# Optimization experiments

Hardware: AMD Instinct MI355X
Metric: run time of the kernel (lower is better)

Reference implementation:

```python
import jax, jax.numpy as jnp
import numpy as np

D_MODEL = 1024
D_FF = 4096
N = 16384


def setup_inputs() -> dict:
    key = jax.random.key(0)
    k_b, k_w1, k_b1, k_w2, k_b2 = jax.random.split(key, 5)
    s1 = 1.0 / np.sqrt(D_MODEL)
    s2 = 1.0 / np.sqrt(D_FF)
    return {
        "batch": jax.random.normal(k_b, (N, D_MODEL), dtype=jnp.float32),
        # nn.Linear stores weight as [out_features, in_features]
        "W1": jax.random.uniform(k_w1, (D_FF, D_MODEL), jnp.float32, -s1, s1),
        "b1": jax.random.uniform(k_b1, (D_FF,), jnp.float32, -s1, s1),
        "W2": jax.random.uniform(k_w2, (D_MODEL, D_FF), jnp.float32, -s2, s2),
        "b2": jax.random.uniform(k_b2, (D_MODEL,), jnp.float32, -s2, s2),
    }


def reference(batch, W1, b1, W2, b2):
    # inner = tanh(linear1(batch)) : [N, d_ff]
    inner = jnp.tanh(batch @ W1.T + b1)
    # wx = tanh(linear2(inner)) : [N, d_model]
    wx = jnp.tanh(inner @ W2.T + b2)
    # diag(wx @ batch.T) == row-wise dot product, avoids O(N^2) matmul
    return jax.nn.sigmoid(jnp.sum(wx * batch, axis=-1))  # [N]
```

## Files before the change

### kernel.cpp

```cpp
#include <hip/hip_runtime.h>
#include <math.h>

#define N_ROWS 16384
#define DMODEL 1024
#define DFF    4096

typedef _Float16 f16;
typedef __attribute__((ext_vector_type(4))) _Float16 f16x4;
typedef __attribute__((ext_vector_type(8))) _Float16 f16x8;
typedef __attribute__((ext_vector_type(4))) float f32x4;

__device__ inline void async_ld16(const f16* g, f16* l) {
  __builtin_amdgcn_global_load_lds(
      (__attribute__((address_space(1))) void*)(g),
      (__attribute__((address_space(3))) void*)(l),
      16, 0, 0);
}

__device__ inline float fast_tanh(float x) {
  float t = __expf(2.0f * x);
  return 1.0f - 2.0f / (t + 1.0f);
}

__global__ void cast_to_f16(const float* __restrict__ src, f16* __restrict__ dst, int n) {
  int i = (blockIdx.x * blockDim.x + threadIdx.x) * 8;
  if (i >= n) return;
  float4 v0 = ((const float4*)(src + i))[0];
  float4 v1 = ((const float4*)(src + i))[1];
  f16x8 h = { (f16)v0.x, (f16)v0.y, (f16)v0.z, (f16)v0.w,
              (f16)v1.x, (f16)v1.y, (f16)v1.z, (f16)v1.w };
  *(f16x8*)(dst + i) = h;
}

template <int K>
__global__ __launch_bounds__(256, 3)
void gemm_bt_tanh(const f16* __restrict__ A, const f16* __restrict__ B,
                  const float* __restrict__ bias, f16* __restrict__ C, int Nc) {
  __shared__ __align__(16) f16 As[2 * 128 * 32];
  __shared__ __align__(16) f16 Bs[2 * 128 * 32];

  const int tid  = threadIdx.x;
  const int lane = tid & 63;
  const int wave = tid >> 6;
  const size_t row0 = (size_t)blockIdx.x * 128;
  const size_t col0 = (size_t)blockIdx.y * 128;
  const int wm = (wave >> 1) * 64;
  const int wn = (wave & 1) * 64;
  const int fr = lane & 15;
  const int fk = (lane >> 4) * 8;

  const f16* Ag[4]; const f16* Bg[4]; f16* Asd[4]; f16* Bsd[4];
#pragma unroll
  for (int l = 0; l < 4; ++l) {
    const int sp  = (l & 1) * 256 + tid;
    const int row = sp >> 2;
    const int kch = (l >> 1) * 4 + (sp & 3);
    Ag[l]  = A + (row0 + row) * (size_t)K + kch * 8;
    Bg[l]  = B + (col0 + row) * (size_t)K + kch * 8;
    Asd[l] = As + (l >> 1) * 4096 + sp * 8;
    Bsd[l] = Bs + (l >> 1) * 4096 + sp * 8;
  }

  f32x4 acc[4][4] = {};

  for (int k0 = 0; k0 < K; k0 += 64) {
    __syncthreads();
#pragma unroll
    for (int l = 0; l < 4; ++l) async_ld16(Ag[l] + k0, Asd[l]);
#pragma unroll
    for (int l = 0; l < 4; ++l) async_ld16(Bg[l] + k0, Bsd[l]);
    __syncthreads();

#pragma unroll
    for (int s = 0; s < 2; ++s) {
      f16x8 af[4], bf[4];
#pragma unroll
      for (int i = 0; i < 4; ++i) {
        af[i] = *(const f16x8*)(As + s * 4096 + (wm + i * 16 + fr) * 32 + fk);
        bf[i] = *(const f16x8*)(Bs + s * 4096 + (wn + i * 16 + fr) * 32 + fk);
      }
#pragma unroll
      for (int i = 0; i < 4; ++i)
#pragma unroll
        for (int j = 0; j < 4; ++j)
          acc[i][j] = __builtin_amdgcn_mfma_f32_16x16x32_f16(af[i], bf[j], acc[i][j], 0, 0, 0);
    }
  }

  const int erow = wm + (lane >> 4) * 4;
  const int ecol = wn + fr;
#pragma unroll
  for (int i = 0; i < 4; ++i) {
#pragma unroll
    for (int j = 0; j < 4; ++j) {
      size_t gcol = col0 + ecol + j * 16;
      float b = bias[gcol];
#pragma unroll
      for (int r = 0; r < 4; ++r) {
        size_t grow = row0 + erow + i * 16 + r;
        C[grow * (size_t)Nc + gcol] = (f16)fast_tanh(acc[i][j][r] + b);
      }
    }
  }
}

__global__ void rowdot_sigmoid(const f16* __restrict__ wx, const float* __restrict__ batch,
                               float* __restrict__ out) {
  const int row = blockIdx.x;
  const int t = threadIdx.x;
  const f16* wr = wx + (size_t)row * DMODEL + t * 4;
  const float* br = batch + (size_t)row * DMODEL + t * 4;
  f16x4 h = *(const f16x4*)wr;
  float4 b4 = *(const float4*)br;
  float s = (float)h[0] * b4.x + (float)h[1] * b4.y + (float)h[2] * b4.z + (float)h[3] * b4.w;
#pragma unroll
  for (int off = 32; off > 0; off >>= 1) s += __shfl_down(s, off, 64);
  __shared__ float partial[4];
  if ((t & 63) == 0) partial[t >> 6] = s;
  __syncthreads();
  if (t == 0) {
    float tot = partial[0] + partial[1] + partial[2] + partial[3];
    out[row] = 1.0f / (1.0f + __expf(-tot));
  }
}

extern "C" void kernel_launch(void* const* d_in, const int* in_sizes, int n_in,
                              void* d_out, int out_size, void* d_ws, size_t ws_size,
                              hipStream_t stream) {
  const float* batch = (const float*)d_in[0];
  const float* W1    = (const float*)d_in[1];
  const float* b1    = (const float*)d_in[2];
  const float* W2    = (const float*)d_in[3];
  const float* b2    = (const float*)d_in[4];
  float* out = (float*)d_out;

  char* ws = (char*)d_ws;
  f16* batch_h = (f16*)ws;  ws += (size_t)N_ROWS * DMODEL * sizeof(f16);
  f16* W1_h    = (f16*)ws;  ws += (size_t)DFF * DMODEL * sizeof(f16);
  f16* W2_h    = (f16*)ws;  ws += (size_t)DMODEL * DFF * sizeof(f16);
  f16* inner_h = (f16*)ws;  ws += (size_t)N_ROWS * DFF * sizeof(f16);
  f16* wx_h    = (f16*)ws;  ws += (size_t)N_ROWS * DMODEL * sizeof(f16);

  const int nb = N_ROWS * DMODEL;
  const int nw = DFF * DMODEL;
  cast_to_f16<<<nb / 2048, 256, 0, stream>>>(batch, batch_h, nb);
  cast_to_f16<<<nw / 2048, 256, 0, stream>>>(W1, W1_h, nw);
  cast_to_f16<<<nw / 2048, 256, 0, stream>>>(W2, W2_h, nw);

  dim3 g1(N_ROWS / 128, DFF / 128);
  gemm_bt_tanh<DMODEL><<<g1, 256, 0, stream>>>(batch_h, W1_h, b1, inner_h, DFF);
  dim3 g2(N_ROWS / 128, DMODEL / 128);
  gemm_bt_tanh<DFF><<<g2, 256, 0, stream>>>(inner_h, W2_h, b2, wx_h, DMODEL);

  rowdot_sigmoid<<<N_ROWS, 256, 0, stream>>>(wx_h, batch, out);
}
```

Baseline: 474.4 us.

## Rewrite GEMM as 256x256 tile, 8-wave, swizzled-LDS pipelined kernel

Replaces the 128x128 four-wave GEMM with a 256x256 tile computed by eight waves, using 128 KB of dynamic LDS as a two-stage buffer. Prefetches land two k-steps ahead and are interleaved with MFMA phases. Barriers and setprio stagger the phases, LDS columns are XOR-swizzled to avoid bank conflicts, and the workgroup order is remapped for L2 locality. The aim is more data reuse per tile and hiding global-load latency. In exchange it holds far more registers per wave and may run fewer resident workgroups. Its hand-written waitcnt and barrier choreography could also break correctness if the counts are wrong.

```diff
diff --git a/kernel.cpp b/kernel.cpp
--- a/kernel.cpp
+++ b/kernel.cpp
@@ -32,74 +32,146 @@
   *(f16x8*)(dst + i) = h;
 }
 
+#define BARRIER() asm volatile("s_barrier" ::: "memory")
+
 template <int K>
-__global__ __launch_bounds__(256, 3)
-void gemm_bt_tanh(const f16* __restrict__ A, const f16* __restrict__ B,
+__global__ __launch_bounds__(512, 2)
+void gemm256_tanh(const f16* __restrict__ A, const f16* __restrict__ B,
                   const float* __restrict__ bias, f16* __restrict__ C, int Nc) {
-  __shared__ __align__(16) f16 As[2 * 128 * 32];
-  __shared__ __align__(16) f16 Bs[2 * 128 * 32];
+  extern __shared__ __align__(16) char smem[];
+  f16* lds = (f16*)smem;
 
   const int tid  = threadIdx.x;
   const int lane = tid & 63;
   const int wave = tid >> 6;
-  const size_t row0 = (size_t)blockIdx.x * 128;
-  const size_t col0 = (size_t)blockIdx.y * 128;
-  const int wm = (wave >> 1) * 64;
-  const int wn = (wave & 1) * 64;
+  const int wm = (wave >> 2) * 128;
+  const int wn = (wave & 3) * 64;
   const int fr = lane & 15;
-  const int fk = (lane >> 4) * 8;
-
-  const f16* Ag[4]; const f16* Bg[4]; f16* Asd[4]; f16* Bsd[4];
-#pragma unroll
-  for (int l = 0; l < 4; ++l) {
-    const int sp  = (l & 1) * 256 + tid;
-    const int row = sp >> 2;
-    const int kch = (l >> 1) * 4 + (sp & 3);
-    Ag[l]  = A + (row0 + row) * (size_t)K + kch * 8;
-    Bg[l]  = B + (col0 + row) * (size_t)K + kch * 8;
-    Asd[l] = As + (l >> 1) * 4096 + sp * 8;
-    Bsd[l] = Bs + (l >> 1) * 4096 + sp * 8;
-  }
-
-  f32x4 acc[4][4] = {};
-
-  for (int k0 = 0; k0 < K; k0 += 64) {
-    __syncthreads();
-#pragma unroll
-    for (int l = 0; l < 4; ++l) async_ld16(Ag[l] + k0, Asd[l]);
-#pragma unroll
-    for (int l = 0; l < 4; ++l) async_ld16(Bg[l] + k0, Bsd[l]);
-    __syncthreads();
-
-#pragma unroll
-    for (int s = 0; s < 2; ++s) {
-      f16x8 af[4], bf[4];
-#pragma unroll
-      for (int i = 0; i < 4; ++i) {
-        af[i] = *(const f16x8*)(As + s * 4096 + (wm + i * 16 + fr) * 32 + fk);
-        bf[i] = *(const f16x8*)(Bs + s * 4096 + (wn + i * 16 + fr) * 32 + fk);
-      }
-#pragma unroll
-      for (int i = 0; i < 4; ++i)
-#pragma unroll
-        for (int j = 0; j < 4; ++j)
-          acc[i][j] = __builtin_amdgcn_mfma_f32_16x16x32_f16(af[i], bf[j], acc[i][j], 0, 0, 0);
+  const int g  = lane >> 4;
+  const int kxor = (fr & 7) << 4;
+  const int cb0 = (g * 16) ^ kxor;
+  const int cb1 = (64 + g * 16) ^ kxor;
+
+  const int nbx = gridDim.x;
+  const int nwg = nbx * gridDim.y;
+  const int lin = blockIdx.y * nbx + blockIdx.x;
+  const int swz = (lin & 7) * (nwg >> 3) + (lin >> 3);
+  const size_t row0 = (size_t)(swz % nbx) * 256;
+  const size_t col0 = (size_t)(swz / nbx) * 256;
+
+  const int srow  = tid >> 3;
+  const int sslot = (tid & 7) ^ (srow & 7);
+  const f16* Ag[4]; const f16* Bg[4];
+  int ldA[4], ldB[4];
+#pragma unroll
+  for (int q = 0; q < 4; ++q) {
+    const int row = q * 64 + srow;
+    Ag[q] = A + (row0 + row) * (size_t)K + sslot * 8;
+    Bg[q] = B + (col0 + row) * (size_t)K + sslot * 8;
+    const int c = q * 512 + tid;
+    ldA[q] = c * 8;
+    ldB[q] = 16384 + c * 8;
+  }
+
+  f32x4 acc[8][4] = {};
+  constexpr int NT = K / 64;
+
+#pragma unroll
+  for (int q = 0; q < 4; ++q) {
+    async_ld16(Ag[q], lds + ldA[q]);
+    async_ld16(Bg[q], lds + ldB[q]);
+  }
+#pragma unroll
+  for (int q = 0; q < 4; ++q) {
+    async_ld16(Ag[q] + 64, lds + 32768 + ldA[q]);
+    async_ld16(Bg[q] + 64, lds + 32768 + ldB[q]);
+  }
+  asm volatile("s_waitcnt vmcnt(8)" ::: "memory");
+  BARRIER();
+
+#pragma unroll 2
+  for (int t = 0; t < NT; ++t) {
+    const char* Ts = smem + (t & 1) * 65536;
+    const char* Us = Ts + 32768;
+    f16* sd = lds + (t & 1) * 32768;
+    const int kpre = (t + 2) * 64;
+    const bool pre = (t + 2) < NT;
+
+    f16x8 a0[8], a1[8], b0[4], b1[4];
+#pragma unroll
+    for (int m = 0; m < 8; ++m)
+      a0[m] = *(const f16x8*)(Ts + (wm + m * 16 + fr) * 128 + cb0);
+#pragma unroll
+    for (int n = 0; n < 4; ++n)
+      b0[n] = *(const f16x8*)(Us + (wn + n * 16 + fr) * 128 + cb0);
+    BARRIER();
+    __builtin_amdgcn_s_setprio(1);
+#pragma unroll
+    for (int m = 0; m < 4; ++m)
+#pragma unroll
+      for (int n = 0; n < 4; ++n)
+        acc[m][n] = __builtin_amdgcn_mfma_f32_16x16x32_f16(a0[m], b0[n], acc[m][n], 0, 0, 0);
+    __builtin_amdgcn_s_setprio(0);
+    BARRIER();
+#pragma unroll
+    for (int m = 0; m < 8; ++m)
+      a1[m] = *(const f16x8*)(Ts + (wm + m * 16 + fr) * 128 + cb1);
+#pragma unroll
+    for (int n = 0; n < 4; ++n)
+      b1[n] = *(const f16x8*)(Us + (wn + n * 16 + fr) * 128 + cb1);
+    BARRIER();
+    __builtin_amdgcn_s_setprio(1);
+#pragma unroll
+    for (int m = 4; m < 8; ++m)
+#pragma unroll
+      for (int n = 0; n < 4; ++n)
+        acc[m][n] = __builtin_amdgcn_mfma_f32_16x16x32_f16(a0[m], b0[n], acc[m][n], 0, 0, 0);
+    __builtin_amdgcn_s_setprio(0);
+    asm volatile("s_waitcnt lgkmcnt(0)" ::: "memory");
+    BARRIER();
+    if (pre) {
+      async_ld16(Ag[0] + kpre, sd + ldA[0]);
+      async_ld16(Bg[0] + kpre, sd + ldB[0]);
+      async_ld16(Ag[1] + kpre, sd + ldA[1]);
+      async_ld16(Bg[1] + kpre, sd + ldB[1]);
     }
-  }
-
-  const int erow = wm + (lane >> 4) * 4;
-  const int ecol = wn + fr;
-#pragma unroll
-  for (int i = 0; i < 4; ++i) {
-#pragma unroll
-    for (int j = 0; j < 4; ++j) {
-      size_t gcol = col0 + ecol + j * 16;
-      float b = bias[gcol];
-#pragma unroll
-      for (int r = 0; r < 4; ++r) {
-        size_t grow = row0 + erow + i * 16 + r;
-        C[grow * (size_t)Nc + gcol] = (f16)fast_tanh(acc[i][j][r] + b);
-      }
+    BARRIER();
+    __builtin_amdgcn_s_setprio(1);
+#pragma unroll
+    for (int m = 0; m < 4; ++m)
+#pragma unroll
+      for (int n = 0; n < 4; ++n)
+        acc[m][n] = __builtin_amdgcn_mfma_f32_16x16x32_f16(a1[m], b1[n], acc[m][n], 0, 0, 0);
+    __builtin_amdgcn_s_setprio(0);
+    BARRIER();
+    if (pre) {
+      async_ld16(Ag[2] + kpre, sd + ldA[2]);
+      async_ld16(Bg[2] + kpre, sd + ldB[2]);
+      async_ld16(Ag[3] + kpre, sd + ldA[3]);
+      async_ld16(Bg[3] + kpre, sd + ldB[3]);
+    }
+    __builtin_amdgcn_s_setprio(1);
+#pragma unroll
+    for (int m = 4; m < 8; ++m)
+#pragma unroll
+      for (int n = 0; n < 4; ++n)
+        acc[m][n] = __builtin_amdgcn_mfma_f32_16x16x32_f16(a1[m], b1[n], acc[m][n], 0, 0, 0);
+    __builtin_amdgcn_s_setprio(0);
+    if (pre) asm volatile("s_waitcnt vmcnt(8)" ::: "memory");
+    else     asm volatile("s_waitcnt vmcnt(0)" ::: "memory");
+    BARRIER();
+  }
+
+#pragma unroll
+  for (int m = 0; m < 8; ++m) {
+#pragma unroll
+    for (int n = 0; n < 4; ++n) {
+      const size_t gcol = col0 + wn + n * 16 + fr;
+      const float bia = bias[gcol];
+      f16* Cp = C + (row0 + wm + m * 16 + g * 4) * (size_t)Nc + gcol;
+#pragma unroll
+      for (int r = 0; r < 4; ++r)
+        Cp[(size_t)r * Nc] = (f16)fast_tanh(acc[m][n][r] + bia);
     }
   }
 }
@@ -141,16 +213,25 @@
   f16* inner_h = (f16*)ws;  ws += (size_t)N_ROWS * DFF * sizeof(f16);
   f16* wx_h    = (f16*)ws;  ws += (size_t)N_ROWS * DMODEL * sizeof(f16);
 
+  static bool attr_set = false;
+  if (!attr_set) {
+    (void)hipFuncSetAttribute((const void*)gemm256_tanh<DMODEL>,
+                              hipFuncAttributeMaxDynamicSharedMemorySize, 131072);
+    (void)hipFuncSetAttribute((const void*)gemm256_tanh<DFF>,
+                              hipFuncAttributeMaxDynamicSharedMemorySize, 131072);
+    attr_set = true;
+  }
+
   const int nb = N_ROWS * DMODEL;
   const int nw = DFF * DMODEL;
   cast_to_f16<<<nb / 2048, 256, 0, stream>>>(batch, batch_h, nb);
   cast_to_f16<<<nw / 2048, 256, 0, stream>>>(W1, W1_h, nw);
   cast_to_f16<<<nw / 2048, 256, 0, stream>>>(W2, W2_h, nw);
 
-  dim3 g1(N_ROWS / 128, DFF / 128);
-  gemm_bt_tanh<DMODEL><<<g1, 256, 0, stream>>>(batch_h, W1_h, b1, inner_h, DFF);
-  dim3 g2(N_ROWS / 128, DMODEL / 128);
-  gemm_bt_tanh<DFF><<<g2, 256, 0, stream>>>(inner_h, W2_h, b2, wx_h, DMODEL);
+  dim3 g1(N_ROWS / 256, DFF / 256);
+  gemm256_tanh<DMODEL><<<g1, 512, 131072, stream>>>(batch_h, W1_h, b1, inner_h, DFF);
+  dim3 g2(N_ROWS / 256, DMODEL / 256);
+  gemm256_tanh<DFF><<<g2, 512, 131072, stream>>>(inner_h, W2_h, b2, wx_h, DMODEL);
 
   rowdot_sigmoid<<<N_ROWS, 256, 0, stream>>>(wx_h, batch, out);
 }
```

Measured after the change: 682.6 us. 43.9% more time.
